# Kernel tuning notes

Measured on AMD Instinct MI355X. Metric: run time of the kernel, lower is better.

## Reference

```python
import jax, jax.numpy as jnp
import numpy as np

D_MODEL = 1024
N_HEAD = 16
D_HEAD = D_MODEL // N_HEAD
B, S = 4, 2048


def setup_inputs() -> dict:
    key = jax.random.key(0)
    ks = jax.random.split(key, 10)
    def xavier(k, shape):
        fan_in, fan_out = shape[1], shape[0]
        limit = np.sqrt(6.0 / (fan_in + fan_out))
        return jax.random.uniform(k, shape, jnp.float32, -limit, limit)
    x = jax.random.normal(ks[0], (B, S, D_MODEL), jnp.float32)
    mask = jnp.tril(jnp.ones((S, S), jnp.int32))[None, None]  # causal [1,1,S,S]
    return {
        "x": x,
        "Wq": xavier(ks[1], (D_MODEL, D_MODEL)), "bq": jnp.zeros((D_MODEL,), jnp.float32),
        "Wk": xavier(ks[2], (D_MODEL, D_MODEL)), "bk": jnp.zeros((D_MODEL,), jnp.float32),
        "Wv": xavier(ks[3], (D_MODEL, D_MODEL)), "bv": jnp.zeros((D_MODEL,), jnp.float32),
        "Wo": xavier(ks[4], (D_MODEL, D_MODEL)), "bo": jnp.zeros((D_MODEL,), jnp.float32),
        "mask": mask,
    }


def reference(x, Wq, bq, Wk, bk, Wv, bv, Wo, bo, mask):
    b, s, d = x.shape
    # Linear layers use y = x @ W.T + b (torch convention)
    def proj(W, bias):
        y = jnp.einsum('bsd,ed->bse', x, W) + bias
        return y.reshape(b, s, N_HEAD, D_HEAD).transpose(0, 2, 1, 3)  # [B,H,S,Dh]
    q = proj(Wq, bq)
    k = proj(Wk, bk)
    v = proj(Wv, bv)
    scores = jnp.einsum('bhqd,bhkd->bhqk', q, k) / jnp.sqrt(jnp.float32(D_HEAD))
    scores = jnp.where(mask == 0, jnp.float32(-1e9), scores)
    attn = jax.nn.softmax(scores, axis=-1)  # dropout is identity at eval
    context = jnp.einsum('bhqk,bhkd->bhqd', attn, v)
    context = context.transpose(0, 2, 1, 3).reshape(b, s, d)
    return jnp.einsum('bsd,ed->bse', context, Wo) + bo
```

## Files before the change

kernel.cpp:

```cpp
#include <hip/hip_runtime.h>
#include <stdint.h>

#define D_MODEL 1024
#define NHEAD   16
#define DHEAD   64
#define BATCH   4
#define SEQ     2048
#define MTOT    (BATCH*SEQ)

typedef __attribute__((ext_vector_type(4)))  float f32x4;
typedef __attribute__((ext_vector_type(8)))  short bf16x8;

typedef __attribute__((address_space(3))) uint32_t lds_u32;
typedef const __attribute__((address_space(1))) uint32_t glb_u32;

__device__ static inline void gload_lds16(const void* g, void* l) {
    __builtin_amdgcn_global_load_lds((glb_u32*)g, (lds_u32*)l, 16, 0, 0);
}

__device__ static inline ushort f2bf(float f) {
    uint32_t u = __builtin_bit_cast(uint32_t, f);
    u += 0x7fffu + ((u >> 16) & 1u);
    return (ushort)(u >> 16);
}

__device__ static inline float exp2_fast(float x) {
    float r; asm("v_exp_f32 %0, %1" : "=v"(r) : "v"(x)); return r;
}
__device__ static inline uint32_t cvt_pk_bf16(float a, float b) {
    uint32_t r;
    asm("v_cvt_pk_bf16_f32 %0, %1, %2" : "=v"(r) : "v"(a), "v"(b));
    return r;
}

__global__ __launch_bounds__(256) void convert_kernel(
    const float4* __restrict__ x,
    const float4* __restrict__ wq, const float4* __restrict__ wk,
    const float4* __restrict__ wv, const float4* __restrict__ wo,
    ushort4* __restrict__ xb, ushort4* __restrict__ wb)
{
    const int NX4 = (MTOT * D_MODEL) / 4;
    const int NW4 = (D_MODEL * D_MODEL) / 4;
    const int TOT = NX4 + 4 * NW4;
    for (int i = blockIdx.x * blockDim.x + threadIdx.x; i < TOT;
         i += gridDim.x * blockDim.x) {
        float4 v; ushort4* dst;
        if (i < NX4) { v = x[i]; dst = &xb[i]; }
        else {
            int j = i - NX4;
            int w = j >> 18;
            int r = j & (NW4 - 1);
            const float4* s = (w == 0) ? wq : (w == 1) ? wk : (w == 2) ? wv : wo;
            v = s[r]; dst = &wb[(size_t)w * NW4 + r];
        }
        ushort4 o;
        o.x = f2bf(v.x); o.y = f2bf(v.y); o.z = f2bf(v.z); o.w = f2bf(v.w);
        *dst = o;
    }
}


#define GEMM8_BODY(APTR, BPTR, NKT)                                         \
    __shared__ __align__(16) ushort S[3 * 24576];  \
    const int tid = threadIdx.x;                                            \
    const int w = tid >> 6, l = tid & 63;                                   \
    const int lo = l & 15, hi = l >> 4;                        \
    const int wm = w >> 1, wn = w & 1;                                      \
    const int srA = w * 8 + (l >> 3);                 \
    const int sgA = l & 7;                             \
    f32x4 acc[4][4] = {};                                                   \
    auto stageA2 = [&](int buf, int kt, int j0) {                           \
        ushort* SA = &S[buf * 24576];                                       \
        _Pragma("unroll")                                                   \
        for (int j = j0; j < j0 + 2; ++j) {                                 \
            const int row = j * 64 + srA;                                   \
            const int g = sgA ^ (row & 7);                                  \
            gload_lds16((APTR) + (size_t)(m0 + row) * 1024 + kt * 64 + g * 8,\
                        SA + (j * 64 + w * 8) * 64);                        \
        }                                                                   \
    };                                                                      \
    auto stageB2 = [&](int buf, int kt) {                                   \
        ushort* SB = &S[buf * 24576] + 16384;                               \
        _Pragma("unroll")                                                   \
        for (int j = 0; j < 2; ++j) {                                       \
            const int row = j * 64 + srA;                                   \
            const int g = sgA ^ (row & 7);                                  \
            gload_lds16((BPTR) + (size_t)(n0 + row) * 1024 + kt * 64 + g * 8,\
                        SB + (j * 64 + w * 8) * 64);                        \
        }                                                                   \
    };                                                                      \
             \
    stageA2(0, 0, 0); stageA2(0, 0, 2); stageB2(0, 0);                      \
    stageA2(1, 1, 0); stageA2(1, 1, 2); stageB2(1, 1);                      \
    asm volatile("s_waitcnt vmcnt(6)" ::: "memory");                        \
    __builtin_amdgcn_s_barrier();                                           \
    __builtin_amdgcn_sched_barrier(0);                                      \
    int cur = 0;                                                            \
    for (int kt = 0; kt < (NKT); ++kt) {                                    \
        const int stg = (cur + 2 >= 3) ? cur - 1 : cur + 2;                 \
        const char* SA = (const char*)&S[cur * 24576];                      \
        const char* SB = SA + 32768;                                        \
        const bool doStage = (kt + 2 < (NKT));                              \
        _Pragma("unroll")                                                   \
        for (int p = 0; p < 4; ++p) {                                       \
            bf16x8 af[2][2], bf[2][2];                                      \
            _Pragma("unroll")                                               \
            for (int mi = 0; mi < 2; ++mi)                                  \
                _Pragma("unroll")                                           \
                for (int ks = 0; ks < 2; ++ks) {                            \
                    const int ar = wm * 64 + (p >> 1) * 32 + mi * 16 + lo;  \
                    const int ga = (ks * 4 + hi) ^ (ar & 7);                \
                    af[mi][ks] = *(const bf16x8*)(SA + ar * 128 + ga * 16); \
                    const int bc = wn * 64 + (p & 1) * 32 + mi * 16 + lo;   \
                    const int gb = (ks * 4 + hi) ^ (bc & 7);                \
                    bf[mi][ks] = *(const bf16x8*)(SB + bc * 128 + gb * 16); \
                }                                                           \
            if (doStage) {                                                  \
                if (p == 0)      stageA2(stg, kt + 2, 0);                   \
                else if (p == 1) stageA2(stg, kt + 2, 2);                   \
                else if (p == 2) stageB2(stg, kt + 2);                      \
            }                                                               \
            __builtin_amdgcn_s_barrier();                                   \
            asm volatile("s_waitcnt lgkmcnt(0)" ::: "memory");              \
            __builtin_amdgcn_sched_barrier(0);                              \
            __builtin_amdgcn_s_setprio(1);                                  \
            _Pragma("unroll")                                               \
            for (int ks = 0; ks < 2; ++ks)                                  \
                _Pragma("unroll")                                           \
                for (int mi = 0; mi < 2; ++mi)                              \
                    _Pragma("unroll")                                       \
                    for (int ni = 0; ni < 2; ++ni)                          \
                        acc[(p >> 1) * 2 + mi][(p & 1) * 2 + ni] =          \
                            __builtin_amdgcn_mfma_f32_16x16x32_bf16(        \
                                af[mi][ks], bf[ni][ks],                     \
                                acc[(p >> 1) * 2 + mi][(p & 1) * 2 + ni],   \
                                0, 0, 0);                                   \
            __builtin_amdgcn_s_setprio(0);                                  \
            if (p == 3) {                                                   \
                if (kt + 2 < (NKT))                                         \
                    { asm volatile("s_waitcnt vmcnt(6)" ::: "memory"); }    \
                else if (kt + 2 == (NKT))                                   \
                    { asm volatile("s_waitcnt vmcnt(0)" ::: "memory"); }    \
            }                                                               \
            __builtin_amdgcn_s_barrier();                                   \
            __builtin_amdgcn_sched_barrier(0);                              \
        }                                                                   \
        cur = (cur == 2) ? 0 : cur + 1;                                     \
    }

__global__ __launch_bounds__(512, 1) void gemm_qkv(
    const ushort* __restrict__ A,
    const ushort* __restrict__ W3,
    const float* __restrict__ bq, const float* __restrict__ bk,
    const float* __restrict__ bv,
    ushort* __restrict__ Qb, ushort* __restrict__ Kb, ushort* __restrict__ Vtb,
    float qscale)
{
    const int id = blockIdx.x;
    const int xcd = id & 7, q = id >> 3;
    const int mb = xcd * 4 + (q & 3);
    const int nb = q >> 2;
    const int m0 = mb * 256, n0 = nb * 128;

    GEMM8_BODY(A, W3, 16)

    const int region = nb >> 3;
    const float scale = (region == 0) ? qscale : 1.0f;
    const float* bias = (region == 0) ? bq : (region == 1) ? bk : bv;
    ushort* outQK = (region == 0) ? Qb : Kb;

#pragma unroll
    for (int mi = 0; mi < 4; ++mi) {
#pragma unroll
        for (int ni = 0; ni < 4; ++ni) {
            const int gj  = n0 + wn * 64 + ni * 16 + lo;
            const int lcl = gj & 1023;
            const int h = lcl >> 6, dh = lcl & 63;
            const float bj = bias[lcl];
            const int gi0 = m0 + wm * 64 + mi * 16 + hi * 4;
            const int b = gi0 >> 11, s0 = gi0 & (SEQ - 1);
            if (region < 2) {
#pragma unroll
                for (int r = 0; r < 4; ++r)
                    outQK[(((size_t)(b * NHEAD + h)) * SEQ + s0 + r) * DHEAD + dh] =
                        f2bf((acc[mi][ni][r] + bj) * scale);
            } else {
                ushort4 o4;
                o4.x = f2bf(acc[mi][ni][0] + bj);
                o4.y = f2bf(acc[mi][ni][1] + bj);
                o4.z = f2bf(acc[mi][ni][2] + bj);
                o4.w = f2bf(acc[mi][ni][3] + bj);
                *(ushort4*)&Vtb[(((size_t)(b * NHEAD + h)) * DHEAD + dh) * SEQ + s0] = o4;
            }
        }
    }
}

__global__ __launch_bounds__(512, 1) void gemm_out(
    const ushort* __restrict__ A,
    const ushort* __restrict__ W,
    const float*  __restrict__ bias,
    float* __restrict__ out)
{
    const int id = blockIdx.x;
    const int xcd = id & 7, q = id >> 3;
    const int mb = xcd * 4 + (q & 3);
    const int nb = q >> 2;
    const int m0 = mb * 256, n0 = nb * 128;

    GEMM8_BODY(A, W, 16)

#pragma unroll
    for (int mi = 0; mi < 4; ++mi)
#pragma unroll
        for (int ni = 0; ni < 4; ++ni) {
            const int gj = n0 + wn * 64 + ni * 16 + lo;
            const float bj = bias[gj];
            const int gi0 = m0 + wm * 64 + mi * 16 + hi * 4;
#pragma unroll
            for (int r = 0; r < 4; ++r)
                out[(size_t)(gi0 + r) * D_MODEL + gj] = acc[mi][ni][r] + bj;
        }
}

__global__ __launch_bounds__(256) void attn_kernel(
    const ushort* __restrict__ Q, const ushort* __restrict__ K,
    const ushort* __restrict__ Vt, ushort* __restrict__ ctx)
{
    __shared__ __align__(16) ushort Ks[64 * 64];
    __shared__ __align__(16) ushort Vs[64 * 64];
    __shared__ __align__(16) ushort Pq[4 * 32 * 64];

    const int tid = threadIdx.x;
    const int w = tid >> 6, l = tid & 63, lo = l & 15, hi = l >> 4;
    const int sw = lo & 7;

    const int fid = blockIdx.x;
    const int xcd = fid & 7;
    const int u = fid >> 3;
    const int g = xcd * 8 + (u & 7);
    const int b = g >> 4, h = g & 15;
    const int j = u >> 3;
    const size_t base = (size_t)(b * NHEAD + h) * SEQ * DHEAD;

    const int krow = tid >> 3;
    const int kcol = (tid & 7) * 8;
    char* PqW = (char*)&Pq[w * 2048];

    for (int pass = 0; pass < 2; ++pass) {
        const int qt = pass ? (15 - j) : j;
        const int q0 = qt << 7;
        const int qw0 = q0 + w * 32;

        bf16x8 qf[2][2];
#pragma unroll
        for (int mi = 0; mi < 2; ++mi)
#pragma unroll
            for (int ks = 0; ks < 2; ++ks)
                qf[mi][ks] = *(const bf16x8*)&Q[base +
                    (size_t)(qw0 + mi * 16 + lo) * DHEAD + ks * 32 + hi * 8];

        f32x4 o[2][4] = {};
        float mrow[2] = {-1e30f, -1e30f}, lrow[2] = {0.f, 0.f};

        const int ntiles = (q0 + 128) >> 6;

        bf16x8 kregA[2], vregA[2], kregB[2], vregB[2];
#pragma unroll
        for (int c = 0; c < 2; ++c) {
            kregA[c] = *(const bf16x8*)&K[base + (size_t)(c * 32 + krow) * DHEAD + kcol];
            vregA[c] = *(const bf16x8*)&Vt[base + (size_t)(c * 32 + krow) * SEQ + kcol];
            kregB[c] = *(const bf16x8*)&K[base + (size_t)(64 + c * 32 + krow) * DHEAD + kcol];
            vregB[c] = *(const bf16x8*)&Vt[base + (size_t)(c * 32 + krow) * SEQ + 64 + kcol];
        }

        auto tile_body = [&](int t, bf16x8 (&KR)[2], bf16x8 (&VR)[2]) {
            const int kv0 = t << 6;
            __syncthreads();
#pragma unroll
            for (int c = 0; c < 2; ++c) {
                const int row = c * 32 + krow;
                const int g16 = (tid & 7) ^ (row & 7);
                *(bf16x8*)((char*)Ks + row * 128 + (g16 << 4)) = KR[c];
                *(bf16x8*)((char*)Vs + row * 128 + (g16 << 4)) = VR[c];
            }
            __syncthreads();
            if (t + 2 < ntiles) {
                const int nv0 = kv0 + 128;
#pragma unroll
                for (int c = 0; c < 2; ++c) {
                    KR[c] = *(const bf16x8*)&K[base + (size_t)(nv0 + c * 32 + krow) * DHEAD + kcol];
                    VR[c] = *(const bf16x8*)&Vt[base + (size_t)(c * 32 + krow) * SEQ + nv0 + kcol];
                }
            }
            if (kv0 > qw0 + 31) return;

            f32x4 s[2][4] = {};
            __builtin_amdgcn_s_setprio(1);
#pragma unroll
            for (int ks = 0; ks < 2; ++ks) {
                bf16x8 kf[4];
#pragma unroll
                for (int nj = 0; nj < 4; ++nj)
                    kf[nj] = *(const bf16x8*)((char*)Ks + (nj * 16 + lo) * 128 +
                                              ((((ks << 2) + hi) ^ sw) << 4));
#pragma unroll
                for (int mi = 0; mi < 2; ++mi)
#pragma unroll
                    for (int nj = 0; nj < 4; ++nj)
                        s[mi][nj] = __builtin_amdgcn_mfma_f32_16x16x32_bf16(
                            kf[nj], qf[mi][ks], s[mi][nj], 0, 0, 0);
            }
            __builtin_amdgcn_s_setprio(0);

            if (kv0 + 63 > qw0) {
#pragma unroll
                for (int mi = 0; mi < 2; ++mi) {
                    const int gq = qw0 + mi * 16 + lo;
#pragma unroll
                    for (int nj = 0; nj < 4; ++nj)
#pragma unroll
                        for (int r = 0; r < 4; ++r) {
                            const int gk = kv0 + nj * 16 + hi * 4 + r;
                            if (gk > gq) s[mi][nj][r] = -1e30f;
                        }
                }
            }

            float tl[2], corr[2];
#pragma unroll
            for (int mi = 0; mi < 2; ++mi) {
                float m = s[mi][0][0];
#pragma unroll
                for (int nj = 0; nj < 4; ++nj)
#pragma unroll
                    for (int r = 0; r < 4; ++r) m = fmaxf(m, s[mi][nj][r]);
                tl[mi] = m;
            }
            const bool grow = (tl[0] > mrow[0] + 8.f) | (tl[1] > mrow[1] + 8.f);
            if (__any(grow)) {
#pragma unroll
                for (int mi = 0; mi < 2; ++mi) {
                    float m2 = fmaxf(tl[mi], __shfl_xor(tl[mi], 16));
                    m2 = fmaxf(m2, __shfl_xor(m2, 32));
                    const float mn = fmaxf(mrow[mi], m2);
                    corr[mi] = exp2_fast(mrow[mi] - mn);
                    mrow[mi] = mn;
                }
#pragma unroll
                for (int mi = 0; mi < 2; ++mi)
#pragma unroll
                    for (int r = 0; r < 4; ++r) {
                        const float cb = __shfl(corr[mi], hi * 4 + r);
#pragma unroll
                        for (int ni = 0; ni < 4; ++ni) o[mi][ni][r] *= cb;
                    }
            } else { corr[0] = 1.f; corr[1] = 1.f; }

#pragma unroll
            for (int mi = 0; mi < 2; ++mi) {
                float ls = 0.f;
#pragma unroll
                for (int nj = 0; nj < 4; ++nj) {
#pragma unroll
                    for (int r = 0; r < 4; ++r) {
                        const float p = exp2_fast(s[mi][nj][r] - mrow[mi]);
                        s[mi][nj][r] = p;
                        ls += p;
                    }
                    uint2 pp;
                    pp.x = cvt_pk_bf16(s[mi][nj][0], s[mi][nj][1]);
                    pp.y = cvt_pk_bf16(s[mi][nj][2], s[mi][nj][3]);
                    const int gP = ((nj << 1) + (hi >> 1)) ^ sw;
                    *(uint2*)(PqW + (mi * 16 + lo) * 128 + (gP << 4) + ((hi & 1) << 3)) = pp;
                }
                ls += __shfl_xor(ls, 16);
                ls += __shfl_xor(ls, 32);
                lrow[mi] = lrow[mi] * corr[mi] + ls;
            }

            __builtin_amdgcn_s_setprio(1);
#pragma unroll
            for (int ks2 = 0; ks2 < 2; ++ks2) {
                bf16x8 pf[2], vf[4];
#pragma unroll
                for (int mi = 0; mi < 2; ++mi)
                    pf[mi] = *(const bf16x8*)(PqW + (mi * 16 + lo) * 128 +
                                              ((((ks2 << 2) + hi) ^ sw) << 4));
#pragma unroll
                for (int ni = 0; ni < 4; ++ni)
                    vf[ni] = *(const bf16x8*)((char*)Vs + (ni * 16 + lo) * 128 +
                                              ((((ks2 << 2) + hi) ^ sw) << 4));
#pragma unroll
                for (int mi = 0; mi < 2; ++mi)
#pragma unroll
                    for (int ni = 0; ni < 4; ++ni)
                        o[mi][ni] = __builtin_amdgcn_mfma_f32_16x16x32_bf16(
                            pf[mi], vf[ni], o[mi][ni], 0, 0, 0);
            }
            __builtin_amdgcn_s_setprio(0);
        };

        for (int tt = 0; tt < ntiles; tt += 2) {
            tile_body(tt,     kregA, vregA);
            tile_body(tt + 1, kregB, vregB);
        }

#pragma unroll
        for (int mi = 0; mi < 2; ++mi) {
            const float rv = 1.0f / lrow[mi];
#pragma unroll
            for (int r = 0; r < 4; ++r) {
                const float rb = __shfl(rv, hi * 4 + r);
                const int gq = qw0 + mi * 16 + hi * 4 + r;
#pragma unroll
                for (int ni = 0; ni < 4; ++ni)
                    ctx[((size_t)(b * SEQ + gq)) * D_MODEL + h * DHEAD + ni * 16 + lo] =
                        f2bf(o[mi][ni][r] * rb);
            }
        }
    }
}

extern "C" void kernel_launch(void* const* d_in, const int* in_sizes, int n_in,
                              void* d_out, int out_size, void* d_ws, size_t ws_size,
                              hipStream_t stream) {
    const float* x  = (const float*)d_in[0];
    const float* Wq = (const float*)d_in[1];
    const float* bq = (const float*)d_in[2];
    const float* Wk = (const float*)d_in[3];
    const float* bk = (const float*)d_in[4];
    const float* Wv = (const float*)d_in[5];
    const float* bv = (const float*)d_in[6];
    const float* Wo = (const float*)d_in[7];
    const float* bo = (const float*)d_in[8];

    char* ws = (char*)d_ws;
    ushort* xb  = (ushort*)(ws);
    ushort* wb  = (ushort*)(ws + (16u << 20));
    ushort* Qb  = (ushort*)(ws + (24u << 20));
    ushort* Kb  = (ushort*)(ws + (40u << 20));
    ushort* Vtb = (ushort*)(ws + (56u << 20));
    ushort* ctx = (ushort*)(ws + (72u << 20));

    convert_kernel<<<2048, 256, 0, stream>>>(
        (const float4*)x, (const float4*)Wq, (const float4*)Wk,
        (const float4*)Wv, (const float4*)Wo, (ushort4*)xb, (ushort4*)wb);

    const int NW = D_MODEL * D_MODEL;
    const float qscale = 0.125f * 1.44269504f;

    gemm_qkv<<<768, 512, 0, stream>>>(xb, wb, bq, bk, bv, Qb, Kb, Vtb, qscale);

    attn_kernel<<<512, 256, 0, stream>>>(Qb, Kb, Vtb, ctx);

    gemm_out<<<256, 512, 0, stream>>>(ctx, wb + 3 * NW, bo, (float*)d_out);
}
```

Measured before the change: 179.3 us.

## Enlarge GEMM tiles to 256x256 with double-buffered LDS pipeline

```diff
diff --git a/kernel.cpp b/kernel.cpp
--- a/kernel.cpp
+++ b/kernel.cpp
@@ -60,95 +60,70 @@
 }
 
 
-#define GEMM8_BODY(APTR, BPTR, NKT)                                         \
-    __shared__ __align__(16) ushort S[3 * 24576];  \
+#define GEMM256_BODY(APTR, BPTR)                                            \
+    __shared__ __align__(16) ushort S[2 * 32768];   \
     const int tid = threadIdx.x;                                            \
     const int w = tid >> 6, l = tid & 63;                                   \
     const int lo = l & 15, hi = l >> 4;                        \
-    const int wm = w >> 1, wn = w & 1;                                      \
-    const int srA = w * 8 + (l >> 3);                 \
-    const int sgA = l & 7;                             \
-    f32x4 acc[4][4] = {};                                                   \
-    auto stageA2 = [&](int buf, int kt, int j0) {                           \
-        ushort* SA = &S[buf * 24576];                                       \
+    const int wm = w >> 2, wn = w & 3;                         \
+    const int sr = l >> 3, sg = l & 7;                                      \
+    f32x4 acc[8][4] = {};                                                   \
+    auto stage = [&](int buf, int kt) {                                     \
+        ushort* SP = &S[buf * 32768];                                       \
         _Pragma("unroll")                                                   \
-        for (int j = j0; j < j0 + 2; ++j) {                                 \
-            const int row = j * 64 + srA;                                   \
-            const int g = sgA ^ (row & 7);                                  \
+        for (int j = 0; j < 4; ++j) {                                       \
+            const int row = w * 32 + j * 8 + sr;                            \
+            const int g = sg ^ sr;                         \
             gload_lds16((APTR) + (size_t)(m0 + row) * 1024 + kt * 64 + g * 8,\
-                        SA + (j * 64 + w * 8) * 64);                        \
+                        SP + (w * 32 + j * 8) * 64);                        \
+            gload_lds16((BPTR) + (size_t)(n0 + row) * 1024 + kt * 64 + g * 8,\
+                        SP + 16384 + (w * 32 + j * 8) * 64);                \
         }                                                                   \
     };                                                                      \
-    auto stageB2 = [&](int buf, int kt) {                                   \
-        ushort* SB = &S[buf * 24576] + 16384;                               \
-        _Pragma("unroll")                                                   \
-        for (int j = 0; j < 2; ++j) {                                       \
-            const int row = j * 64 + srA;                                   \
-            const int g = sgA ^ (row & 7);                                  \
-            gload_lds16((BPTR) + (size_t)(n0 + row) * 1024 + kt * 64 + g * 8,\
-                        SB + (j * 64 + w * 8) * 64);                        \
-        }                                                                   \
-    };                                                                      \
-             \
-    stageA2(0, 0, 0); stageA2(0, 0, 2); stageB2(0, 0);                      \
-    stageA2(1, 1, 0); stageA2(1, 1, 2); stageB2(1, 1);                      \
-    asm volatile("s_waitcnt vmcnt(6)" ::: "memory");                        \
+    stage(0, 0);                                                            \
+    asm volatile("s_waitcnt vmcnt(0)" ::: "memory");                        \
     __builtin_amdgcn_s_barrier();                                           \
     __builtin_amdgcn_sched_barrier(0);                                      \
     int cur = 0;                                                            \
-    for (int kt = 0; kt < (NKT); ++kt) {                                    \
-        const int stg = (cur + 2 >= 3) ? cur - 1 : cur + 2;                 \
-        const char* SA = (const char*)&S[cur * 24576];                      \
+    for (int kt = 0; kt < 16; ++kt) {                                       \
+        if (kt + 1 < 16) stage(cur ^ 1, kt + 1);                            \
+        const char* SA = (const char*)&S[cur * 32768];                      \
         const char* SB = SA + 32768;                                        \
-        const bool doStage = (kt + 2 < (NKT));                              \
         _Pragma("unroll")                                                   \
-        for (int p = 0; p < 4; ++p) {                                       \
-            bf16x8 af[2][2], bf[2][2];                                      \
+        for (int ks = 0; ks < 2; ++ks) {                                    \
+            bf16x8 af[8], bfr[4];                                           \
             _Pragma("unroll")                                               \
-            for (int mi = 0; mi < 2; ++mi)                                  \
-                _Pragma("unroll")                                           \
-                for (int ks = 0; ks < 2; ++ks) {                            \
-                    const int ar = wm * 64 + (p >> 1) * 32 + mi * 16 + lo;  \
-                    const int ga = (ks * 4 + hi) ^ (ar & 7);                \
-                    af[mi][ks] = *(const bf16x8*)(SA + ar * 128 + ga * 16); \
-                    const int bc = wn * 64 + (p & 1) * 32 + mi * 16 + lo;   \
-                    const int gb = (ks * 4 + hi) ^ (bc & 7);                \
-                    bf[mi][ks] = *(const bf16x8*)(SB + bc * 128 + gb * 16); \
-                }                                                           \
-            if (doStage) {                                                  \
-                if (p == 0)      stageA2(stg, kt + 2, 0);                   \
-                else if (p == 1) stageA2(stg, kt + 2, 2);                   \
-                else if (p == 2) stageB2(stg, kt + 2);                      \
+            for (int mi = 0; mi < 8; ++mi) {                                \
+                const int r = wm * 128 + mi * 16 + lo;                      \
+                af[mi] = *(const bf16x8*)(SA + r * 128 +                    \
+                          (((ks * 4 + hi) ^ (r & 7)) << 4));                \
             }                                                               \
-            __builtin_amdgcn_s_barrier();                                   \
+            _Pragma("unroll")                                               \
+            for (int ni = 0; ni < 4; ++ni) {                                \
+                const int c = wn * 64 + ni * 16 + lo;                       \
+                bfr[ni] = *(const bf16x8*)(SB + c * 128 +                   \
+                          (((ks * 4 + hi) ^ (c & 7)) << 4));                \
+            }                                                               \
             asm volatile("s_waitcnt lgkmcnt(0)" ::: "memory");              \
             __builtin_amdgcn_sched_barrier(0);                              \
             __builtin_amdgcn_s_setprio(1);                                  \
             _Pragma("unroll")                                               \
-            for (int ks = 0; ks < 2; ++ks)                                  \
+            for (int mi = 0; mi < 8; ++mi)                                  \
                 _Pragma("unroll")                                           \
-                for (int mi = 0; mi < 2; ++mi)                              \
-                    _Pragma("unroll")                                       \
-                    for (int ni = 0; ni < 2; ++ni)                          \
-                        acc[(p >> 1) * 2 + mi][(p & 1) * 2 + ni] =          \
-                            __builtin_amdgcn_mfma_f32_16x16x32_bf16(        \
-                                af[mi][ks], bf[ni][ks],                     \
-                                acc[(p >> 1) * 2 + mi][(p & 1) * 2 + ni],   \
-                                0, 0, 0);                                   \
+                for (int ni = 0; ni < 4; ++ni)                              \
+                    acc[mi][ni] = __builtin_amdgcn_mfma_f32_16x16x32_bf16(  \
+                        af[mi], bfr[ni], acc[mi][ni], 0, 0, 0);             \
             __builtin_amdgcn_s_setprio(0);                                  \
-            if (p == 3) {                                                   \
-                if (kt + 2 < (NKT))                                         \
-                    { asm volatile("s_waitcnt vmcnt(6)" ::: "memory"); }    \
-                else if (kt + 2 == (NKT))                                   \
-                    { asm volatile("s_waitcnt vmcnt(0)" ::: "memory"); }    \
-            }                                                               \
+        }                                                                   \
+        if (kt + 1 < 16) {                                                  \
+            asm volatile("s_waitcnt vmcnt(0)" ::: "memory");                \
             __builtin_amdgcn_s_barrier();                                   \
             __builtin_amdgcn_sched_barrier(0);                              \
         }                                                                   \
-        cur = (cur == 2) ? 0 : cur + 1;                                     \
+        cur ^= 1;                                                           \
     }
 
-__global__ __launch_bounds__(512, 1) void gemm_qkv(
+__global__ __launch_bounds__(512) void gemm_qkv(
     const ushort* __restrict__ A,
     const ushort* __restrict__ W3,
     const float* __restrict__ bq, const float* __restrict__ bk,
@@ -160,24 +135,24 @@
     const int xcd = id & 7, q = id >> 3;
     const int mb = xcd * 4 + (q & 3);
     const int nb = q >> 2;
-    const int m0 = mb * 256, n0 = nb * 128;
-
-    GEMM8_BODY(A, W3, 16)
-
-    const int region = nb >> 3;
+    const int m0 = mb * 256, n0 = nb * 256;
+
+    GEMM256_BODY(A, W3)
+
+    const int region = nb >> 2;
     const float scale = (region == 0) ? qscale : 1.0f;
     const float* bias = (region == 0) ? bq : (region == 1) ? bk : bv;
     ushort* outQK = (region == 0) ? Qb : Kb;
 
 #pragma unroll
-    for (int mi = 0; mi < 4; ++mi) {
+    for (int mi = 0; mi < 8; ++mi) {
 #pragma unroll
         for (int ni = 0; ni < 4; ++ni) {
             const int gj  = n0 + wn * 64 + ni * 16 + lo;
             const int lcl = gj & 1023;
             const int h = lcl >> 6, dh = lcl & 63;
             const float bj = bias[lcl];
-            const int gi0 = m0 + wm * 64 + mi * 16 + hi * 4;
+            const int gi0 = m0 + wm * 128 + mi * 16 + hi * 4;
             const int b = gi0 >> 11, s0 = gi0 & (SEQ - 1);
             if (region < 2) {
 #pragma unroll
@@ -196,7 +171,7 @@
     }
 }
 
-__global__ __launch_bounds__(512, 1) void gemm_out(
+__global__ __launch_bounds__(512) void gemm_out(
     const ushort* __restrict__ A,
     const ushort* __restrict__ W,
     const float*  __restrict__ bias,
@@ -206,17 +181,17 @@
     const int xcd = id & 7, q = id >> 3;
     const int mb = xcd * 4 + (q & 3);
     const int nb = q >> 2;
-    const int m0 = mb * 256, n0 = nb * 128;
-
-    GEMM8_BODY(A, W, 16)
-
-#pragma unroll
-    for (int mi = 0; mi < 4; ++mi)
+    const int m0 = mb * 256, n0 = nb * 256;
+
+    GEMM256_BODY(A, W)
+
+#pragma unroll
+    for (int mi = 0; mi < 8; ++mi)
 #pragma unroll
         for (int ni = 0; ni < 4; ++ni) {
             const int gj = n0 + wn * 64 + ni * 16 + lo;
             const float bj = bias[gj];
-            const int gi0 = m0 + wm * 64 + mi * 16 + hi * 4;
+            const int gi0 = m0 + wm * 128 + mi * 16 + hi * 4;
 #pragma unroll
             for (int r = 0; r < 4; ++r)
                 out[(size_t)(gi0 + r) * D_MODEL + gj] = acc[mi][ni][r] + bj;
@@ -450,9 +425,9 @@
     const int NW = D_MODEL * D_MODEL;
     const float qscale = 0.125f * 1.44269504f;
 
-    gemm_qkv<<<768, 512, 0, stream>>>(xb, wb, bq, bk, bv, Qb, Kb, Vtb, qscale);
+    gemm_qkv<<<384, 512, 0, stream>>>(xb, wb, bq, bk, bv, Qb, Kb, Vtb, qscale);
 
     attn_kernel<<<512, 256, 0, stream>>>(Qb, Kb, Vtb, ctx);
 
-    gemm_out<<<256, 512, 0, stream>>>(ctx, wb + 3 * NW, bo, (float*)d_out);
-}
+    gemm_out<<<128, 512, 0, stream>>>(ctx, wb + 3 * NW, bo, (float*)d_out);
+}
```

Result: faster. 172.4 us (-3.9%).
